# Kernel tuning notes

Measured on AMD Instinct MI355X. Metric: run time of the kernel, lower is better.

The kernel has to match this reference:

```python
import jax, jax.numpy as jnp
import numpy as np

D_MODEL, D_STATE, D_CONV, EXPAND = 1024, 16, 4, 2
D_INNER = EXPAND * D_MODEL
EPS = 1e-6


def setup_inputs() -> dict:
    key = jax.random.key(0)
    ks = jax.random.split(key, 8)
    B, T = 2, 1024
    s = lambda fan_in: 1.0 / np.sqrt(fan_in)
    x = jax.random.normal(ks[0], (B, T, D_MODEL), dtype=jnp.float32)
    norm_w = jnp.ones((D_MODEL,), jnp.float32)
    in_proj_w = jax.random.normal(ks[1], (D_MODEL, 2 * D_INNER), jnp.float32) * s(D_MODEL)
    conv_w = jax.random.normal(ks[2], (D_INNER, 1, D_CONV), jnp.float32) * s(D_CONV)
    dt_w = jax.random.normal(ks[3], (D_INNER, D_INNER), jnp.float32) * s(D_INNER)
    dt_b = jnp.zeros((D_INNER,), jnp.float32)
    # A_log init: log(arange(1..d_state)) repeated over d_inner rows
    A_log = jnp.log(jnp.broadcast_to(jnp.arange(1, D_STATE + 1, dtype=jnp.float32), (D_INNER, D_STATE)))
    B_w = jax.random.normal(ks[4], (D_INNER, D_STATE), jnp.float32) * s(D_INNER)
    C_w = jax.random.normal(ks[5], (D_INNER, D_STATE), jnp.float32) * s(D_INNER)
    D_skip = jnp.ones((D_INNER,), jnp.float32)
    out_proj_w = jax.random.normal(ks[6], (D_INNER, D_MODEL), jnp.float32) * s(D_INNER)
    return {"x": x, "norm_w": norm_w, "in_proj_w": in_proj_w, "conv_w": conv_w,
            "dt_w": dt_w, "dt_b": dt_b, "A_log": A_log, "B_w": B_w, "C_w": C_w,
            "D_skip": D_skip, "out_proj_w": out_proj_w}


def _forward(x, norm_w, in_proj_w, conv_w, dt_w, dt_b, A_log, B_w, C_w, D_skip, out_proj_w):
    Bsz, T, _ = x.shape
    # RMSNorm
    xn = x * jax.lax.rsqrt(jnp.mean(x * x, axis=-1, keepdims=True) + EPS) * norm_w
    # in_proj + gated silu
    xg = xn @ in_proj_w                                  # [B,T,2*di]
    x_inner, gate = jnp.split(xg, 2, axis=-1)
    x_inner = x_inner * jax.nn.silu(gate)                # [B,T,di]
    # causal depthwise conv (torch pads both sides then takes first T == left-pad only)
    xc = jax.lax.conv_general_dilated(
        x_inner.transpose(0, 2, 1), conv_w, window_strides=(1,),
        padding=[(D_CONV - 1, 0)], feature_group_count=D_INNER,
        dimension_numbers=("NCH", "OIH", "NCH")).transpose(0, 2, 1)  # [B,T,di]
    dt = jax.nn.softplus(xc @ dt_w + dt_b)               # [B,T,di]
    A = -jnp.exp(A_log)                                  # [di,ds]
    Bm = xc @ B_w                                        # [B,T,ds]
    Cm = xc @ C_w                                        # [B,T,ds]
    A_bar = jnp.exp(dt[..., None] * A)                   # [B,T,di,ds]
    B_bar = dt[..., None] * Bm[:, :, None, :]            # [B,T,di,ds]

    def step(h, inp):
        a_t, b_t, xc_t, c_t = inp                        # [B,di,ds],[B,di,ds],[B,di],[B,ds]
        h = a_t * h + b_t * xc_t[..., None]
        y = jnp.einsum("bds,bs->bd", h, c_t) + D_skip * xc_t
        return h, y

    h0 = jnp.zeros((Bsz, D_INNER, D_STATE), x.dtype)
    xs = (A_bar.transpose(1, 0, 2, 3), B_bar.transpose(1, 0, 2, 3),
          xc.transpose(1, 0, 2), Cm.transpose(1, 0, 2))
    _, ys = jax.lax.scan(step, h0, xs)                   # ys: [T,B,di]
    out = ys.transpose(1, 0, 2) @ out_proj_w             # [B,T,d_model]
    return out


def reference(x, norm_w, in_proj_w, conv_w, dt_w, dt_b, A_log, B_w, C_w, D_skip, out_proj_w):
    return _forward(x, norm_w, in_proj_w, conv_w, dt_w, dt_b, A_log, B_w, C_w, D_skip, out_proj_w)
```

## Files before the change

kernel.cpp:

```cpp
#include <hip/hip_runtime.h>
#include <cmath>


#define SEQ    1024
#define BATCH  2
#define DMODEL 1024
#define DINNER 2048
#define DSTATE 16
#define NTOK   (BATCH * SEQ)
#define NCHUNK 32
#define CLEN   32
#define NEXT   2112

typedef __attribute__((ext_vector_type(8))) short short8;
typedef __attribute__((ext_vector_type(4))) float f32x4;

__device__ __forceinline__ unsigned short f2bf(float f) {
  unsigned int u = __float_as_uint(f);
  unsigned int r = (u + 0x7fffu + ((u >> 16) & 1u)) >> 16;
  return (unsigned short)r;
}
__device__ __forceinline__ float bf2f(unsigned short v) {
  return __uint_as_float((unsigned int)v << 16);
}
__device__ __forceinline__ float softplus_f(float x) {
  return (x > 20.f) ? x : log1pf(__expf(x));
}
__device__ __forceinline__ void gload_lds16(const void* g, void* l) {
  __builtin_amdgcn_global_load_lds(
      (const __attribute__((address_space(1))) unsigned int*)g,
      (__attribute__((address_space(3))) unsigned int*)l, 16, 0, 0);
}

template <int N>
__device__ __forceinline__ void wait_vmcnt() {
  if constexpr (N >= 8)      asm volatile("s_waitcnt vmcnt(8)" ::: "memory");
  else if constexpr (N == 6) asm volatile("s_waitcnt vmcnt(6)" ::: "memory");
  else if constexpr (N == 4) asm volatile("s_waitcnt vmcnt(4)" ::: "memory");
  else                       asm volatile("s_waitcnt vmcnt(0)" ::: "memory");
}

__device__ __forceinline__ size_t tiled_off(int row, int k, int kblks) {
  return ((size_t)(row >> 4) * kblks + (k >> 5)) * 512
       + ((size_t)((row & 15) + (((k >> 3) & 3) << 4)) << 3) + (k & 7);
}

__global__ __launch_bounds__(256) void init_aneg_k(const float* __restrict__ A_log,
                                                   float* __restrict__ Aneg) {
  int i = blockIdx.x * 256 + threadIdx.x;
  Aneg[i] = -__expf(A_log[i]);
}

__global__ void transpose_cvt_k(const float* __restrict__ W, unsigned short* __restrict__ Wt,
                                int K, int N) {
  __shared__ float tile[32][33];
  int k0 = blockIdx.y * 32, n0 = blockIdx.x * 32;
  int tx = threadIdx.x, ty = threadIdx.y;
  int kblks = K >> 5;
#pragma unroll
  for (int i = 0; i < 32; i += 8)
    tile[ty + i][tx] = W[(size_t)(k0 + ty + i) * N + n0 + tx];
  __syncthreads();
#pragma unroll
  for (int i = 0; i < 32; i += 8)
    Wt[tiled_off(n0 + ty + i, k0 + tx, kblks)] = f2bf(tile[tx][ty + i]);
}

__global__ void build_w2t_k(const float* __restrict__ dt_w, const float* __restrict__ B_w,
                            const float* __restrict__ C_w, unsigned short* __restrict__ Wt) {
  __shared__ float tile[32][33];
  int k0 = blockIdx.x * 32, n0 = blockIdx.y * 32;
  int tx = threadIdx.x, ty = threadIdx.y;
  if (n0 < DINNER) {
#pragma unroll
    for (int i = 0; i < 32; i += 8)
      tile[ty + i][tx] = dt_w[(size_t)(k0 + ty + i) * DINNER + n0 + tx];
    __syncthreads();
#pragma unroll
    for (int i = 0; i < 32; i += 8)
      Wt[tiled_off(n0 + ty + i, k0 + tx, 64)] = f2bf(tile[tx][ty + i]);
  } else {
#pragma unroll
    for (int i = 0; i < 32; i += 8) {
      int n = n0 + ty + i;
      float v = 0.f;
      if (n < DINNER + 16) v = B_w[(size_t)(k0 + tx) * DSTATE + (n - DINNER)];
      else if (n < DINNER + 32) v = C_w[(size_t)(k0 + tx) * DSTATE + (n - DINNER - 16)];
      Wt[tiled_off(n, k0 + tx, 64)] = f2bf(v);
    }
  }
}

__global__ __launch_bounds__(256) void rmsnorm_k(const float* __restrict__ x,
                                                 const float* __restrict__ w,
                                                 unsigned short* __restrict__ xnbf) {
  int row = blockIdx.x, tid = threadIdx.x;
  const float4 v = *(const float4*)(x + (size_t)row * DMODEL + tid * 4);
  float ss = v.x * v.x + v.y * v.y + v.z * v.z + v.w * v.w;
#pragma unroll
  for (int off = 32; off > 0; off >>= 1) ss += __shfl_down(ss, off);
  __shared__ float red[4];
  if ((tid & 63) == 0) red[tid >> 6] = ss;
  __syncthreads();
  float tot = red[0] + red[1] + red[2] + red[3];
  float scale = rsqrtf(tot * (1.0f / DMODEL) + 1e-6f);
  const float4 wv = *(const float4*)(w + tid * 4);
  ushort4 o;
  o.x = f2bf(v.x * scale * wv.x);
  o.y = f2bf(v.y * scale * wv.y);
  o.z = f2bf(v.z * scale * wv.z);
  o.w = f2bf(v.w * scale * wv.w);
  *(ushort4*)(xnbf + tiled_off(row, tid * 4, DMODEL / 32)) = o;
}

template <int BM, int BN, int MODE>
__global__ __launch_bounds__(256) void gemm_bf16_t(const unsigned short* __restrict__ At,
                                                   const unsigned short* __restrict__ Btt,
                                                   float* __restrict__ C,
                                                   int M, int N, int K, int ldc,
                                                   const float* __restrict__ bias,
                                                   float* __restrict__ Bm,
                                                   float* __restrict__ Cm) {
  constexpr int WTM = BM / 2, WTN = BN / 2;
  constexpr int FM = WTM / 16, FN = WTN / 16;
  constexpr int ASUB = BM / 16, BSUB = BN / 16;
  constexpr int ALOAD = ASUB * 2, BLOAD = BSUB * 2;
  constexpr int LPW = (BM + BN) / 32;
  __shared__ __align__(16) unsigned short Abuf[2][BM * 64];
  __shared__ __align__(16) unsigned short Bbuf[2][BN * 64];
  const int tid = threadIdx.x;
  const int wave = tid >> 6, lane = tid & 63;

  const int gx = gridDim.x;
  int lin = blockIdx.y * gx + blockIdx.x;
  int nwg = gx * gridDim.y;
  int swz = (lin & 7) * (nwg >> 3) + (lin >> 3);
  const int bm = (swz / gx) * BM, bn = (swz % gx) * BN;

  const int wm = wave >> 1, wn = wave & 1;
  const int kblks = K >> 5;
  const unsigned short* Ag = At + ((size_t)(bm >> 4) * kblks) * 512 + (lane << 3);
  const unsigned short* Bg = Btt + ((size_t)(bn >> 4) * kblks) * 512 + (lane << 3);

  auto stage = [&](int buf, int t) {
#pragma unroll
    for (int i = wave; i < ALOAD; i += 4) {
      int s = i >> 1, kk = i & 1;
      gload_lds16(Ag + ((size_t)s * kblks + 2 * t + kk) * 512,
                  &Abuf[buf][(kk * ASUB + s) * 512]);
    }
#pragma unroll
    for (int i = wave; i < BLOAD; i += 4) {
      int s = i >> 1, kk = i & 1;
      gload_lds16(Bg + ((size_t)s * kblks + 2 * t + kk) * 512,
                  &Bbuf[buf][(kk * BSUB + s) * 512]);
    }
  };

  f32x4 acc[FM][FN] = {};
  const int nt = K / 64;
  stage(0, 0);
  stage(1, 1);
  for (int t = 0; t < nt; ++t) {
    const int cur = t & 1;
    if (t + 1 < nt) wait_vmcnt<LPW>();
    else            wait_vmcnt<0>();
    __builtin_amdgcn_s_barrier();
    short8 af[2][FM], bfr[2][FN];
#pragma unroll
    for (int kk = 0; kk < 2; ++kk) {
#pragma unroll
      for (int m = 0; m < FM; ++m)
        af[kk][m] = *(const short8*)&Abuf[cur][(kk * ASUB + wm * FM + m) * 512 + (lane << 3)];
#pragma unroll
      for (int n = 0; n < FN; ++n)
        bfr[kk][n] = *(const short8*)&Bbuf[cur][(kk * BSUB + wn * FN + n) * 512 + (lane << 3)];
    }
    asm volatile("s_waitcnt lgkmcnt(0)" ::: "memory");
    __builtin_amdgcn_sched_barrier(0);
    __builtin_amdgcn_s_barrier();
    if (t + 2 < nt) stage(cur, t + 2);
#pragma unroll
    for (int kk = 0; kk < 2; ++kk)
#pragma unroll
      for (int m = 0; m < FM; ++m)
#pragma unroll
        for (int n = 0; n < FN; ++n)
          acc[m][n] = __builtin_amdgcn_mfma_f32_16x16x32_bf16(af[kk][m], bfr[kk][n],
                                                              acc[m][n], 0, 0, 0);
  }

  const int rbase = bm + wm * WTM + (lane >> 4) * 4;
  const int cbase = bn + wn * WTN + (lane & 15);
#pragma unroll
  for (int m = 0; m < FM; ++m)
#pragma unroll
    for (int n = 0; n < FN; ++n) {
      int col = cbase + n * 16;
#pragma unroll
      for (int r = 0; r < 4; ++r) {
        int row = rbase + m * 16 + r;
        float v = acc[m][n][r];
        if (MODE == 0) {
          C[(size_t)row * ldc + col] = v;
        } else {
          if (col < DINNER)
            C[(size_t)row * DINNER + col] = softplus_f(v + bias[col]);
          else if (col < DINNER + 16)
            Bm[(size_t)row * DSTATE + (col - DINNER)] = v;
          else if (col < DINNER + 32)
            Cm[(size_t)row * DSTATE + (col - DINNER - 16)] = v;
        }
      }
    }
}

__global__ __launch_bounds__(256) void siluconv_k(const float* __restrict__ xg,
                                                  const float* __restrict__ w,
                                                  unsigned short* __restrict__ xcbf) {
  int idx = blockIdx.x * 256 + threadIdx.x;
  int d4 = (idx & 511) << 2;
  int tc = (idx >> 9) & 127;
  int b = idx >> 16;
  float4 w0 = *(const float4*)(w + (d4 + 0) * 4);
  float4 w1 = *(const float4*)(w + (d4 + 1) * 4);
  float4 w2 = *(const float4*)(w + (d4 + 2) * 4);
  float4 w3 = *(const float4*)(w + (d4 + 3) * 4);
  const float wj0[4] = {w0.x, w0.y, w0.z, w0.w};
  const float wj1[4] = {w1.x, w1.y, w1.z, w1.w};
  const float wj2[4] = {w2.x, w2.y, w2.z, w2.w};
  const float wj3[4] = {w3.x, w3.y, w3.z, w3.w};
  const float* pa = xg + (size_t)b * SEQ * (2 * DINNER) + d4;
  const float* pg = pa + DINNER;
  int t0 = tc * 8;
  float4 sA = {0.f, 0.f, 0.f, 0.f}, sB = sA, sC = sA;
  auto gated = [&](int t) {
    float4 a = *(const float4*)(pa + (size_t)t * (2 * DINNER));
    float4 g = *(const float4*)(pg + (size_t)t * (2 * DINNER));
    float4 r;
    r.x = a.x * (g.x / (1.f + __expf(-g.x)));
    r.y = a.y * (g.y / (1.f + __expf(-g.y)));
    r.z = a.z * (g.z / (1.f + __expf(-g.z)));
    r.w = a.w * (g.w / (1.f + __expf(-g.w)));
    return r;
  };
  if (t0 > 0) {
    sA = gated(t0 - 3);
    sB = gated(t0 - 2);
    sC = gated(t0 - 1);
  }
#pragma unroll
  for (int j = 0; j < 8; ++j) {
    int t = t0 + j;
    float4 sD = gated(t);
    float4 o;
    o.x = sA.x * wj0[0] + sB.x * wj0[1] + sC.x * wj0[2] + sD.x * wj0[3];
    o.y = sA.y * wj1[0] + sB.y * wj1[1] + sC.y * wj1[2] + sD.y * wj1[3];
    o.z = sA.z * wj2[0] + sB.z * wj2[1] + sC.z * wj2[2] + sD.z * wj2[3];
    o.w = sA.w * wj3[0] + sB.w * wj3[1] + sC.w * wj3[2] + sD.w * wj3[3];
    ushort4 ob = {f2bf(o.x), f2bf(o.y), f2bf(o.z), f2bf(o.w)};
    *(ushort4*)(xcbf + tiled_off(b * SEQ + t, d4, 64)) = ob;
    sA = sB; sB = sC; sC = sD;
  }
}

__global__ __launch_bounds__(256) void scan_local_k(const float* __restrict__ dt,
                                                    const unsigned short* __restrict__ xcbf,
                                                    const float* __restrict__ Bm,
                                                    const float* __restrict__ A,
                                                    float* __restrict__ hfin,
                                                    float* __restrict__ P) {
  int d = blockIdx.x * 256 + threadIdx.x;
  int c = blockIdx.y, b = blockIdx.z;
  float a[DSTATE], h[DSTATE];
#pragma unroll
  for (int s = 0; s < DSTATE; ++s) { a[s] = A[(size_t)d * DSTATE + s]; h[s] = 0.f; }
  float sdt = 0.f;
  int t0 = c * CLEN;
  for (int t = t0; t < t0 + CLEN; ++t) {
    size_t ro = (size_t)(b * SEQ + t);
    float dtv = dt[ro * DINNER + d];
    float xv = bf2f(xcbf[tiled_off((int)ro, d, 64)]);
    sdt += dtv;
    float bx = dtv * xv;
    float4 q0 = *(const float4*)(Bm + ro * DSTATE + 0);
    float4 q1 = *(const float4*)(Bm + ro * DSTATE + 4);
    float4 q2 = *(const float4*)(Bm + ro * DSTATE + 8);
    float4 q3 = *(const float4*)(Bm + ro * DSTATE + 12);
    float bm[DSTATE] = {q0.x, q0.y, q0.z, q0.w, q1.x, q1.y, q1.z, q1.w,
                        q2.x, q2.y, q2.z, q2.w, q3.x, q3.y, q3.z, q3.w};
#pragma unroll
    for (int s = 0; s < DSTATE; ++s) {
      float av = __expf(a[s] * dtv);
      h[s] = fmaf(av, h[s], bx * bm[s]);
    }
  }
  size_t o = ((size_t)(b * NCHUNK + c) * DINNER + d) * DSTATE;
#pragma unroll
  for (int s = 0; s < DSTATE; ++s) {
    hfin[o + s] = h[s];
    P[o + s] = __expf(a[s] * sdt);
  }
}

__global__ __launch_bounds__(256) void scan_chunks_k(float* hp, const float* __restrict__ P) {
  int j = blockIdx.x * 256 + threadIdx.x;
  int b = j / (DINNER * DSTATE);
  int r = j % (DINNER * DSTATE);
  float H = 0.f;
  for (int c = 0; c < NCHUNK; ++c) {
    size_t o = ((size_t)(b * NCHUNK + c) * DINNER * DSTATE) + r;
    float hf = hp[o];
    float pv = P[o];
    hp[o] = H;
    H = fmaf(pv, H, hf);
  }
}

__global__ __launch_bounds__(256) void scan_final_k(const float* __restrict__ dt,
                                                    const unsigned short* __restrict__ xcbf,
                                                    const float* __restrict__ Bm,
                                                    const float* __restrict__ Cm,
                                                    const float* __restrict__ A,
                                                    const float* __restrict__ Hprev,
                                                    const float* __restrict__ Dskip,
                                                    unsigned short* __restrict__ ysbf) {
  int d = blockIdx.x * 256 + threadIdx.x;
  int c = blockIdx.y, b = blockIdx.z;
  float a[DSTATE], h[DSTATE];
  size_t ho = ((size_t)(b * NCHUNK + c) * DINNER + d) * DSTATE;
#pragma unroll
  for (int s = 0; s < DSTATE; ++s) {
    a[s] = A[(size_t)d * DSTATE + s];
    h[s] = Hprev[ho + s];
  }
  float Dv = Dskip[d];
  int t0 = c * CLEN;
  for (int t = t0; t < t0 + CLEN; ++t) {
    size_t ro = (size_t)(b * SEQ + t);
    float dtv = dt[ro * DINNER + d];
    float xv = bf2f(xcbf[tiled_off((int)ro, d, 64)]);
    float bx = dtv * xv;
    float4 q0 = *(const float4*)(Bm + ro * DSTATE + 0);
    float4 q1 = *(const float4*)(Bm + ro * DSTATE + 4);
    float4 q2 = *(const float4*)(Bm + ro * DSTATE + 8);
    float4 q3 = *(const float4*)(Bm + ro * DSTATE + 12);
    float bm[DSTATE] = {q0.x, q0.y, q0.z, q0.w, q1.x, q1.y, q1.z, q1.w,
                        q2.x, q2.y, q2.z, q2.w, q3.x, q3.y, q3.z, q3.w};
    float4 r0 = *(const float4*)(Cm + ro * DSTATE + 0);
    float4 r1 = *(const float4*)(Cm + ro * DSTATE + 4);
    float4 r2 = *(const float4*)(Cm + ro * DSTATE + 8);
    float4 r3 = *(const float4*)(Cm + ro * DSTATE + 12);
    float cm[DSTATE] = {r0.x, r0.y, r0.z, r0.w, r1.x, r1.y, r1.z, r1.w,
                        r2.x, r2.y, r2.z, r2.w, r3.x, r3.y, r3.z, r3.w};
    float y = Dv * xv;
#pragma unroll
    for (int s = 0; s < DSTATE; ++s) {
      float av = __expf(a[s] * dtv);
      h[s] = fmaf(av, h[s], bx * bm[s]);
      y = fmaf(h[s], cm[s], y);
    }
    ysbf[tiled_off((int)ro, d, 64)] = f2bf(y);
  }
}

extern "C" void kernel_launch(void* const* d_in, const int* in_sizes, int n_in,
                              void* d_out, int out_size, void* d_ws, size_t ws_size,
                              hipStream_t stream) {
  (void)in_sizes; (void)n_in; (void)out_size; (void)ws_size;
  const float* x       = (const float*)d_in[0];
  const float* norm_w  = (const float*)d_in[1];
  const float* in_proj = (const float*)d_in[2];
  const float* conv_w  = (const float*)d_in[3];
  const float* dt_w    = (const float*)d_in[4];
  const float* dt_b    = (const float*)d_in[5];
  const float* A_log   = (const float*)d_in[6];
  const float* B_w     = (const float*)d_in[7];
  const float* C_w     = (const float*)d_in[8];
  const float* D_skip  = (const float*)d_in[9];
  const float* out_w   = (const float*)d_in[10];
  float* out = (float*)d_out;
  float* ws = (float*)d_ws;

  float* Aneg = ws;
  float* Bm   = ws + 32768;
  float* Cm   = ws + 65536;
  float* b0   = ws + 98304;
  float* xg   = b0;
  float* dtb  = b0;
  float* hfin = b0 + 4194304;
  float* Pbuf = b0 + 6291456;
  unsigned short* xc_bf = (unsigned short*)(b0 + 8388608);
  unsigned short* ys_bf = (unsigned short*)(b0 + 10485760);
  float* Rw   = b0 + 12582912;
  unsigned short* in_wT  = (unsigned short*)Rw;
  unsigned short* W2t    = (unsigned short*)Rw;
  unsigned short* out_wT = (unsigned short*)Rw;
  unsigned short* xn_bf  = (unsigned short*)(b0 + 14745600);

  init_aneg_k<<<dim3(DINNER * DSTATE / 256), dim3(256), 0, stream>>>(A_log, Aneg);
  transpose_cvt_k<<<dim3(2 * DINNER / 32, DMODEL / 32), dim3(32, 8), 0, stream>>>(
      in_proj, in_wT, DMODEL, 2 * DINNER);
  rmsnorm_k<<<dim3(NTOK), dim3(256), 0, stream>>>(x, norm_w, xn_bf);
  gemm_bf16_t<128, 128, 0><<<dim3(2 * DINNER / 128, NTOK / 128), dim3(256), 0, stream>>>(
      xn_bf, in_wT, xg, NTOK, 2 * DINNER, DMODEL, 2 * DINNER, nullptr, nullptr, nullptr);
  siluconv_k<<<dim3(NTOK * (DINNER / 4) / 8 / 256), dim3(256), 0, stream>>>(
      xg, conv_w, xc_bf);
  build_w2t_k<<<dim3(DINNER / 32, NEXT / 32), dim3(32, 8), 0, stream>>>(
      dt_w, B_w, C_w, W2t);
  gemm_bf16_t<128, 64, 2><<<dim3(NEXT / 64, NTOK / 128), dim3(256), 0, stream>>>(
      xc_bf, W2t, dtb, NTOK, NEXT, DINNER, DINNER, dt_b, Bm, Cm);
  scan_local_k<<<dim3(DINNER / 256, NCHUNK, BATCH), dim3(256), 0, stream>>>(
      dtb, xc_bf, Bm, Aneg, hfin, Pbuf);
  scan_chunks_k<<<dim3(BATCH * DINNER * DSTATE / 256), dim3(256), 0, stream>>>(
      hfin, Pbuf);
  scan_final_k<<<dim3(DINNER / 256, NCHUNK, BATCH), dim3(256), 0, stream>>>(
      dtb, xc_bf, Bm, Cm, Aneg, hfin, D_skip, ys_bf);
  transpose_cvt_k<<<dim3(DMODEL / 32, DINNER / 32), dim3(32, 8), 0, stream>>>(
      out_w, out_wT, DINNER, DMODEL);
  gemm_bf16_t<64, 64, 0><<<dim3(DMODEL / 64, NTOK / 64), dim3(256), 0, stream>>>(
      ys_bf, out_wT, out, NTOK, DMODEL, DINNER, DMODEL, nullptr, nullptr, nullptr);
}
```

Before: 178.7 us.

## Store in_proj output as bf16, retune GEMM wave layouts and tile sizes

The in_proj GEMM now writes its output as bf16 instead of fp32, and the silu-conv kernel reads bf16. This halves the traffic of the largest intermediate tensor. The GEMM template gains configurable wave grids: the first two GEMMs use 8 waves (512 threads) and the out_proj GEMM uses 64x32 tiles for more workgroups. The block swizzle is changed to be M-major, and the vmcnt waits are generalized. Rounding xg to bf16 adds precision loss before the gated silu.

```diff
diff --git a/kernel.cpp b/kernel.cpp
--- a/kernel.cpp
+++ b/kernel.cpp
@@ -34,10 +34,14 @@
 
 template <int N>
 __device__ __forceinline__ void wait_vmcnt() {
-  if constexpr (N >= 8)      asm volatile("s_waitcnt vmcnt(8)" ::: "memory");
+  if constexpr (N <= 0)      asm volatile("s_waitcnt vmcnt(0)" ::: "memory");
+  else if constexpr (N == 1) asm volatile("s_waitcnt vmcnt(1)" ::: "memory");
+  else if constexpr (N == 2) asm volatile("s_waitcnt vmcnt(2)" ::: "memory");
+  else if constexpr (N == 3) asm volatile("s_waitcnt vmcnt(3)" ::: "memory");
+  else if constexpr (N == 4) asm volatile("s_waitcnt vmcnt(4)" ::: "memory");
+  else if constexpr (N == 5) asm volatile("s_waitcnt vmcnt(5)" ::: "memory");
   else if constexpr (N == 6) asm volatile("s_waitcnt vmcnt(6)" ::: "memory");
-  else if constexpr (N == 4) asm volatile("s_waitcnt vmcnt(4)" ::: "memory");
-  else                       asm volatile("s_waitcnt vmcnt(0)" ::: "memory");
+  else                       asm volatile("s_waitcnt vmcnt(8)" ::: "memory");
 }
 
 __device__ __forceinline__ size_t tiled_off(int row, int k, int kblks) {
@@ -113,44 +117,43 @@
   *(ushort4*)(xnbf + tiled_off(row, tid * 4, DMODEL / 32)) = o;
 }
 
-template <int BM, int BN, int MODE>
-__global__ __launch_bounds__(256) void gemm_bf16_t(const unsigned short* __restrict__ At,
-                                                   const unsigned short* __restrict__ Btt,
-                                                   float* __restrict__ C,
-                                                   int M, int N, int K, int ldc,
-                                                   const float* __restrict__ bias,
-                                                   float* __restrict__ Bm,
-                                                   float* __restrict__ Cm) {
-  constexpr int WTM = BM / 2, WTN = BN / 2;
+template <int BM, int BN, int WM, int WN, int MODE>
+__global__ __launch_bounds__(WM * WN * 64) void gemm_bf16_t(
+    const unsigned short* __restrict__ At, const unsigned short* __restrict__ Btt,
+    void* __restrict__ Cv, int M, int N, int K, int ldc,
+    const float* __restrict__ bias, float* __restrict__ Bm, float* __restrict__ Cm) {
+  constexpr int NW = WM * WN;
+  constexpr int WTM = BM / WM, WTN = BN / WN;
   constexpr int FM = WTM / 16, FN = WTN / 16;
   constexpr int ASUB = BM / 16, BSUB = BN / 16;
   constexpr int ALOAD = ASUB * 2, BLOAD = BSUB * 2;
-  constexpr int LPW = (BM + BN) / 32;
+  constexpr int LPW = (ALOAD + BLOAD) / NW;
+  static_assert(ALOAD % NW == 0 && BLOAD % NW == 0, "uniform load split");
   __shared__ __align__(16) unsigned short Abuf[2][BM * 64];
   __shared__ __align__(16) unsigned short Bbuf[2][BN * 64];
   const int tid = threadIdx.x;
   const int wave = tid >> 6, lane = tid & 63;
 
-  const int gx = gridDim.x;
-  int lin = blockIdx.y * gx + blockIdx.x;
-  int nwg = gx * gridDim.y;
+  int lin = blockIdx.x + blockIdx.y * gridDim.x;
+  int nwg = gridDim.x * gridDim.y;
   int swz = (lin & 7) * (nwg >> 3) + (lin >> 3);
-  const int bm = (swz / gx) * BM, bn = (swz % gx) * BN;
-
-  const int wm = wave >> 1, wn = wave & 1;
+  const int MT = gridDim.y;
+  const int bm = (swz % MT) * BM, bn = (swz / MT) * BN;
+
+  const int wm = wave / WN, wn = wave % WN;
   const int kblks = K >> 5;
   const unsigned short* Ag = At + ((size_t)(bm >> 4) * kblks) * 512 + (lane << 3);
   const unsigned short* Bg = Btt + ((size_t)(bn >> 4) * kblks) * 512 + (lane << 3);
 
   auto stage = [&](int buf, int t) {
 #pragma unroll
-    for (int i = wave; i < ALOAD; i += 4) {
+    for (int i = wave; i < ALOAD; i += NW) {
       int s = i >> 1, kk = i & 1;
       gload_lds16(Ag + ((size_t)s * kblks + 2 * t + kk) * 512,
                   &Abuf[buf][(kk * ASUB + s) * 512]);
     }
 #pragma unroll
-    for (int i = wave; i < BLOAD; i += 4) {
+    for (int i = wave; i < BLOAD; i += NW) {
       int s = i >> 1, kk = i & 1;
       gload_lds16(Bg + ((size_t)s * kblks + 2 * t + kk) * 512,
                   &Bbuf[buf][(kk * BSUB + s) * 512]);
@@ -202,10 +205,12 @@
         int row = rbase + m * 16 + r;
         float v = acc[m][n][r];
         if (MODE == 0) {
-          C[(size_t)row * ldc + col] = v;
+          ((float*)Cv)[(size_t)row * ldc + col] = v;
+        } else if (MODE == 1) {
+          ((unsigned short*)Cv)[(size_t)row * ldc + col] = f2bf(v);
         } else {
           if (col < DINNER)
-            C[(size_t)row * DINNER + col] = softplus_f(v + bias[col]);
+            ((float*)Cv)[(size_t)row * DINNER + col] = softplus_f(v + bias[col]);
           else if (col < DINNER + 16)
             Bm[(size_t)row * DSTATE + (col - DINNER)] = v;
           else if (col < DINNER + 32)
@@ -215,7 +220,7 @@
     }
 }
 
-__global__ __launch_bounds__(256) void siluconv_k(const float* __restrict__ xg,
+__global__ __launch_bounds__(256) void siluconv_k(const unsigned short* __restrict__ xg,
                                                   const float* __restrict__ w,
                                                   unsigned short* __restrict__ xcbf) {
   int idx = blockIdx.x * 256 + threadIdx.x;
@@ -230,18 +235,19 @@
   const float wj1[4] = {w1.x, w1.y, w1.z, w1.w};
   const float wj2[4] = {w2.x, w2.y, w2.z, w2.w};
   const float wj3[4] = {w3.x, w3.y, w3.z, w3.w};
-  const float* pa = xg + (size_t)b * SEQ * (2 * DINNER) + d4;
-  const float* pg = pa + DINNER;
+  const unsigned short* pa = xg + (size_t)b * SEQ * (2 * DINNER) + d4;
+  const unsigned short* pg = pa + DINNER;
   int t0 = tc * 8;
   float4 sA = {0.f, 0.f, 0.f, 0.f}, sB = sA, sC = sA;
   auto gated = [&](int t) {
-    float4 a = *(const float4*)(pa + (size_t)t * (2 * DINNER));
-    float4 g = *(const float4*)(pg + (size_t)t * (2 * DINNER));
+    ushort4 av = *(const ushort4*)(pa + (size_t)t * (2 * DINNER));
+    ushort4 gv = *(const ushort4*)(pg + (size_t)t * (2 * DINNER));
     float4 r;
-    r.x = a.x * (g.x / (1.f + __expf(-g.x)));
-    r.y = a.y * (g.y / (1.f + __expf(-g.y)));
-    r.z = a.z * (g.z / (1.f + __expf(-g.z)));
-    r.w = a.w * (g.w / (1.f + __expf(-g.w)));
+    float gx = bf2f(gv.x), gy = bf2f(gv.y), gz = bf2f(gv.z), gw = bf2f(gv.w);
+    r.x = bf2f(av.x) * (gx / (1.f + __expf(-gx)));
+    r.y = bf2f(av.y) * (gy / (1.f + __expf(-gy)));
+    r.z = bf2f(av.z) * (gz / (1.f + __expf(-gz)));
+    r.w = bf2f(av.w) * (gw / (1.f + __expf(-gw)));
     return r;
   };
   if (t0 > 0) {
@@ -386,7 +392,7 @@
   float* Bm   = ws + 32768;
   float* Cm   = ws + 65536;
   float* b0   = ws + 98304;
-  float* xg   = b0;
+  unsigned short* xg = (unsigned short*)b0;
   float* dtb  = b0;
   float* hfin = b0 + 4194304;
   float* Pbuf = b0 + 6291456;
@@ -402,13 +408,13 @@
   transpose_cvt_k<<<dim3(2 * DINNER / 32, DMODEL / 32), dim3(32, 8), 0, stream>>>(
       in_proj, in_wT, DMODEL, 2 * DINNER);
   rmsnorm_k<<<dim3(NTOK), dim3(256), 0, stream>>>(x, norm_w, xn_bf);
-  gemm_bf16_t<128, 128, 0><<<dim3(2 * DINNER / 128, NTOK / 128), dim3(256), 0, stream>>>(
+  gemm_bf16_t<128, 128, 2, 4, 1><<<dim3(2 * DINNER / 128, NTOK / 128), dim3(512), 0, stream>>>(
       xn_bf, in_wT, xg, NTOK, 2 * DINNER, DMODEL, 2 * DINNER, nullptr, nullptr, nullptr);
   siluconv_k<<<dim3(NTOK * (DINNER / 4) / 8 / 256), dim3(256), 0, stream>>>(
       xg, conv_w, xc_bf);
   build_w2t_k<<<dim3(DINNER / 32, NEXT / 32), dim3(32, 8), 0, stream>>>(
       dt_w, B_w, C_w, W2t);
-  gemm_bf16_t<128, 64, 2><<<dim3(NEXT / 64, NTOK / 128), dim3(256), 0, stream>>>(
+  gemm_bf16_t<128, 64, 4, 2, 2><<<dim3(NEXT / 64, NTOK / 128), dim3(512), 0, stream>>>(
       xc_bf, W2t, dtb, NTOK, NEXT, DINNER, DINNER, dt_b, Bm, Cm);
   scan_local_k<<<dim3(DINNER / 256, NCHUNK, BATCH), dim3(256), 0, stream>>>(
       dtb, xc_bf, Bm, Aneg, hfin, Pbuf);
@@ -418,6 +424,6 @@
       dtb, xc_bf, Bm, Cm, Aneg, hfin, D_skip, ys_bf);
   transpose_cvt_k<<<dim3(DMODEL / 32, DINNER / 32), dim3(32, 8), 0, stream>>>(
       out_w, out_wT, DINNER, DMODEL);
-  gemm_bf16_t<64, 64, 0><<<dim3(DMODEL / 64, NTOK / 64), dim3(256), 0, stream>>>(
+  gemm_bf16_t<64, 32, 2, 2, 0><<<dim3(DMODEL / 32, NTOK / 64), dim3(256), 0, stream>>>(
       ys_bf, out_wT, out, NTOK, DMODEL, DINNER, DMODEL, nullptr, nullptr, nullptr);
 }
```

New measurement: 174.3 us. -2.5%, faster.
